# Kernel optimization log

Hardware: AMD Instinct MI355X
Metric: run time of the kernel (lower is better)

## Reference

```python
import jax, jax.numpy as jnp
import numpy as np

L, B, D, H, M, F = 384, 16, 1024, 16, 64, 4096
HD = D // H
LEFT, RIGHT = 64, 64
STD_SCALE = 0.5
LN_EPS = 1e-5


def layer_norm(x, w, b):
    mu = jnp.mean(x, axis=-1, keepdims=True)
    var = jnp.mean((x - mu) ** 2, axis=-1, keepdims=True)
    return (x - mu) / jnp.sqrt(var + LN_EPS) * w + b


def linear(x, w, b):  # torch nn.Linear: y = x @ W^T + b, w is [out, in]
    return x @ w.T + b


def attention_suppression(aw, scale):
    # aw: [N, Tq, Tk] raw logits (may contain -inf)
    p = jax.nn.softmax(aw, axis=-1)
    nz = p > 0.0  # entries with -inf logits are exactly 0 after softmax
    nzs = jnp.sum(nz.astype(aw.dtype), axis=-1, keepdims=True)
    mean = jnp.sum(p, axis=-1, keepdims=True) / nzs
    dis = jnp.where(nz, (p - mean) ** 2, jnp.zeros_like(p))
    var = jnp.sum(dis, axis=-1, keepdims=True) / (nzs - 1.0)
    thr = mean - scale * jnp.sqrt(var)
    return jnp.where(p < thr, -jnp.inf, aw)


def setup_inputs() -> dict:
    key = jax.random.key(0)
    ks = jax.random.split(key, 24)
    s = 0.02

    def w(k, shape):
        return jax.random.normal(k, shape, dtype=jnp.float32) * s

    return {
        "x": jax.random.normal(ks[0], (L, B, D), dtype=jnp.float32),
        "memory": jax.random.normal(ks[1], (M, B, D), dtype=jnp.float32),
        "q_w": w(ks[2], (D, D)), "q_b": jnp.zeros((D,), jnp.float32),
        "k_w": w(ks[3], (D, D)), "k_b": jnp.zeros((D,), jnp.float32),
        "v_w": w(ks[4], (D, D)), "v_b": jnp.zeros((D,), jnp.float32),
        "out_w": w(ks[5], (D, D)), "out_b": jnp.zeros((D,), jnp.float32),
        "ln1_w": jnp.ones((D,), jnp.float32), "ln1_b": jnp.zeros((D,), jnp.float32),
        "fc1_w": w(ks[6], (F, D)), "fc1_b": jnp.zeros((F,), jnp.float32),
        "fc2_w": w(ks[7], (D, F)), "fc2_b": jnp.zeros((D,), jnp.float32),
        "ln2_w": jnp.ones((D,), jnp.float32), "ln2_b": jnp.zeros((D,), jnp.float32),
    }


def reference(x, memory, q_w, q_b, k_w, k_b, v_w, v_b, out_w, out_b,
              ln1_w, ln1_b, fc1_w, fc1_b, fc2_w, fc2_b, ln2_w, ln2_b):
    residual = x
    xn = layer_norm(x, ln1_w, ln1_b)  # normalize_before
    # summarization query = mean over segment (excluding left/right context)
    summary = jnp.mean(xn[LEFT:L - RIGHT], axis=0, keepdims=True)  # [1,B,D]
    inp = jnp.concatenate([xn, summary], axis=0)  # [L+1, B, D]
    mem_and_inp = jnp.concatenate([memory, inp[:-1]], axis=0)  # [M+L, B, D]

    scaling = HD ** -0.5
    q = linear(inp, q_w, q_b) * scaling
    k = linear(mem_and_inp, k_w, k_b)
    v = linear(mem_and_inp, v_w, v_b)

    def split_heads(t):  # [T,B,D] -> [B*H, T, HD]
        return t.reshape(t.shape[0], B * H, HD).transpose(1, 0, 2)

    q, k, v = split_heads(q), split_heads(k), split_heads(v)
    aw = jnp.einsum('nqd,nkd->nqk', q, k)  # [B*H, L+1, M+L]
    # disable mem-on-mem: summary (last) query must not attend to memory keys
    aw = aw.at[:, -1, :M].set(-jnp.inf)
    aw = attention_suppression(aw, STD_SCALE)
    p = jax.nn.softmax(aw, axis=-1)
    attn = jnp.einsum('nqk,nkd->nqd', p, v)  # [B*H, L+1, HD]
    attn = attn.transpose(1, 0, 2).reshape(L + 1, B, D)
    out_and_mem = linear(attn, out_w, out_b)
    # next_m = out_and_mem[-1:] appended to state (identity squash); output drops it
    out = out_and_mem[:-1]

    x = residual + out
    residual = x
    xn = layer_norm(x, ln2_w, ln2_b)
    h = jax.nn.relu(linear(xn, fc1_w, fc1_b))
    h = linear(h, fc2_w, fc2_b)
    return residual + h
```

## Files before the change

### kernel.cpp

```cpp
#include <hip/hip_runtime.h>

typedef __bf16 bf16x8 __attribute__((ext_vector_type(8)));
typedef float f32x4 __attribute__((ext_vector_type(4)));
typedef unsigned short u16x8 __attribute__((ext_vector_type(8)));

__device__ __forceinline__ unsigned short f2bf(float f) {
  union { float f; unsigned int u; } v; v.f = f;
  unsigned int r = v.u + 0x7fffu + ((v.u >> 16) & 1u);
  return (unsigned short)(r >> 16);
}

__device__ __forceinline__ void async16(const unsigned short* g, unsigned short* l) {
  __builtin_amdgcn_global_load_lds(
      (const __attribute__((address_space(1))) unsigned int*)g,
      (__attribute__((address_space(3))) unsigned int*)l, 16, 0, 0);
}

__global__ void cvt_all(const float* __restrict__ q_w, const float* __restrict__ k_w,
                        const float* __restrict__ v_w, const float* __restrict__ o_w,
                        const float* __restrict__ f1w, const float* __restrict__ f2w,
                        const float* __restrict__ mem,
                        const float* __restrict__ q_b, const float* __restrict__ k_b,
                        const float* __restrict__ v_b,
                        unsigned short* __restrict__ WQ, unsigned short* __restrict__ WK,
                        unsigned short* __restrict__ WV, unsigned short* __restrict__ WO,
                        unsigned short* __restrict__ WF1, unsigned short* __restrict__ WF2,
                        unsigned short* __restrict__ MEMB, float* __restrict__ QKVB) {
  const int bid = blockIdx.x;
  const float* src; unsigned short* dst; float scale = 1.f; int base;
  if (bid < 1024)       { src = q_w; dst = WQ;  scale = 0.125f; base = 0; }
  else if (bid < 2048)  { src = k_w; dst = WK;  base = 1024; }
  else if (bid < 3072)  { src = v_w; dst = WV;  base = 2048; }
  else if (bid < 4096)  { src = o_w; dst = WO;  base = 3072; }
  else if (bid < 8192)  { src = f1w; dst = WF1; base = 4096; }
  else if (bid < 12288) { src = f2w; dst = WF2; base = 8192; }
  else if (bid < 13312) { src = mem; dst = MEMB; base = 12288; }
  else {
    const int i = (bid - 13312) * 256 + threadIdx.x;
    QKVB[i] = (i < 1024) ? q_b[i] * 0.125f : (i < 2048 ? k_b[i - 1024] : v_b[i - 2048]);
    return;
  }
  const int i = (bid - base) * 256 + threadIdx.x;
  float4 v = ((const float4*)src)[i];
  ushort4 o;
  o.x = f2bf(v.x * scale); o.y = f2bf(v.y * scale);
  o.z = f2bf(v.z * scale); o.w = f2bf(v.w * scale);
  ((ushort4*)dst)[i] = o;
}

template <int PREFILL>
__global__ __launch_bounds__(256) void ln_bf16(
    const float* __restrict__ src, unsigned short* __restrict__ dst,
    const float* __restrict__ g, const float* __restrict__ be,
    const float* __restrict__ fbias, float* __restrict__ dout) {
  const int row = blockIdx.x, tid = threadIdx.x;
  const float4 v = ((const float4*)(src + (size_t)row * 1024))[tid];
  if (PREFILL) {
    const float4 fb = ((const float4*)fbias)[tid];
    float4 r;
    r.x = v.x + fb.x; r.y = v.y + fb.y; r.z = v.z + fb.z; r.w = v.w + fb.w;
    ((float4*)(dout + (size_t)row * 1024))[tid] = r;
  }
  float s = v.x + v.y + v.z + v.w;
  float qq = v.x * v.x + v.y * v.y + v.z * v.z + v.w * v.w;
#pragma unroll
  for (int off = 32; off; off >>= 1) { s += __shfl_xor(s, off); qq += __shfl_xor(qq, off); }
  __shared__ float ps[4], pq[4];
  const int w = tid >> 6, lane = tid & 63;
  if (lane == 0) { ps[w] = s; pq[w] = qq; }
  __syncthreads();
  if (tid == 0) { ps[0] = ps[0] + ps[1] + ps[2] + ps[3]; pq[0] = pq[0] + pq[1] + pq[2] + pq[3]; }
  __syncthreads();
  const float mu = ps[0] * (1.f / 1024.f);
  const float var = pq[0] * (1.f / 1024.f) - mu * mu;
  const float rs = rsqrtf(var + 1e-5f);
  const float4 gv = ((const float4*)g)[tid];
  const float4 bv = ((const float4*)be)[tid];
  ushort4 o;
  o.x = f2bf((v.x - mu) * rs * gv.x + bv.x);
  o.y = f2bf((v.y - mu) * rs * gv.y + bv.y);
  o.z = f2bf((v.z - mu) * rs * gv.z + bv.z);
  o.w = f2bf((v.w - mu) * rs * gv.w + bv.w);
  ((ushort4*)(dst + (size_t)row * 1024))[tid] = o;
}

#define KOFF 6291456ull
#define VOFF 13631488ull
template <int EPI>
__global__ __launch_bounds__(256) void gemm_bt(
    const unsigned short* __restrict__ A, const unsigned short* __restrict__ Bw,
    const float* __restrict__ bias, const float* __restrict__ resid,
    void* __restrict__ Cout, int M, int N, int K, int lda, int ldb, int NBN, int WM) {
  __shared__ __align__(16) unsigned short lA[128 * 32];
  __shared__ __align__(16) unsigned short lB[128 * 32];
  const int tid = threadIdx.x;
  const int w = tid >> 6, lane = tid & 63;
  const int lr = lane & 15, lq = lane >> 4;
  const int l = blockIdx.x;
  const int xcd = l & 7, r = l >> 3;
  const int bm = xcd * WM + (r % WM);
  const int rest = r / WM;
  const int bn = rest % NBN;
  const size_t koff = (size_t)(rest / NBN) * K;
  const unsigned short* Ab = A + (size_t)bm * 128 * lda + koff;
  const unsigned short* Bb = Bw + (size_t)bn * 128 * ldb + koff;
  const int wm = (w & 1) << 6, wn = (w >> 1) << 6;
  f32x4 acc[4][4] = {};
  const int kiters = K >> 5;
  const int c0 = tid, c1 = 256 + tid;
  const int r0 = c0 >> 2, o0 = (c0 & 3) << 3;
  const int r1 = c1 >> 2, o1 = (c1 & 3) << 3;
  for (int kt = 0; kt < kiters; ++kt) {
    const int kb = kt << 5;
    __syncthreads();
    async16(Ab + (size_t)r0 * lda + kb + o0, lA + c0 * 8);
    async16(Bb + (size_t)r0 * ldb + kb + o0, lB + c0 * 8);
    async16(Ab + (size_t)r1 * lda + kb + o1, lA + c1 * 8);
    async16(Bb + (size_t)r1 * ldb + kb + o1, lB + c1 * 8);
    __syncthreads();
    bf16x8 af[4], bfr[4];
#pragma unroll
    for (int i = 0; i < 4; ++i) af[i] = *(const bf16x8*)(lA + (wm + i * 16 + lr) * 32 + lq * 8);
#pragma unroll
    for (int i = 0; i < 4; ++i) bfr[i] = *(const bf16x8*)(lB + (wn + i * 16 + lr) * 32 + lq * 8);
#pragma unroll
    for (int i = 0; i < 4; ++i)
#pragma unroll
      for (int j = 0; j < 4; ++j)
        acc[i][j] = __builtin_amdgcn_mfma_f32_16x16x32_bf16(af[i], bfr[j], acc[i][j], 0, 0, 0);
  }
  const int which = (bn * 128) >> 10;
#pragma unroll
  for (int i = 0; i < 4; ++i) {
#pragma unroll
    for (int j = 0; j < 4; ++j) {
      const int colg = bn * 128 + wn + j * 16 + lr;
      const float bi = (EPI == 6) ? 0.f : bias[colg];
      const int rowg0 = bm * 128 + wm + i * 16 + lq * 4;
#pragma unroll
      for (int r2 = 0; r2 < 4; ++r2) {
        const int rowg = rowg0 + r2;
        const float val = acc[i][j][r2] + bi;
        if (EPI == 5) {
          const int t = rowg >> 4, bb = rowg & 15;
          const int hh = (colg >> 6) & 15, dd = colg & 63;
          const size_t nn = (size_t)(bb * 16 + hh);
          unsigned short* q16 = (unsigned short*)Cout;
          if (which == 0) {
            if (rowg >= 1024) q16[(nn * 384 + (t - 64)) * 64 + dd] = f2bf(val);
          } else if (which == 1) {
            q16[KOFF + (nn * 448 + t) * 64 + dd] = f2bf(val);
          } else {
            q16[VOFF + (nn * 448 + t) * 64 + dd] = f2bf(val);
          }
        } else {
          const size_t idx = (size_t)rowg * N + colg;
          if (EPI == 2) ((float*)Cout)[idx] = val + resid[idx];
          else if (EPI == 3) ((unsigned short*)Cout)[idx] = f2bf(fmaxf(val, 0.f));
          else if (EPI == 6) atomicAdd(&((float*)Cout)[idx], acc[i][j][r2]);
        }
      }
    }
  }
}

__global__ __launch_bounds__(256) void vtrans(const unsigned short* __restrict__ vb,
                                              unsigned short* __restrict__ vt) {
  __shared__ __align__(16) unsigned short ls[64][80];
  const int kc = blockIdx.x, n = blockIdx.y;
  const int tid = threadIdx.x;
#pragma unroll
  for (int i = 0; i < 2; ++i) {
    const int c = i * 256 + tid;
    const int kk = c >> 3, dc = (c & 7) << 3;
    u16x8 val = *(const u16x8*)(vb + ((size_t)n * 448 + kc * 64 + kk) * 64 + dc);
    *(u16x8*)&ls[kk][dc] = val;
  }
  __syncthreads();
#pragma unroll
  for (int i = 0; i < 2; ++i) {
    const int c = i * 256 + tid;
    const int d = c >> 3, kx = (c & 7) << 3;
    u16x8 o;
#pragma unroll
    for (int j = 0; j < 8; ++j) o[j] = ls[kx + j][d];
    *(u16x8*)(vt + ((size_t)n * 64 + d) * 448 + kc * 64 + kx) = o;
  }
}

#define PST 468
__global__ __launch_bounds__(256) void attn_kernel(
    const unsigned short* __restrict__ qt_, const unsigned short* __restrict__ kt_,
    const unsigned short* __restrict__ vt_, unsigned short* __restrict__ attn) {
  __shared__ __align__(16) unsigned short P[16 * PST];
  __shared__ float Rm[4][16], Rs[4][16], Rc[4][16], Rv[4][16], R2[4][16];
  __shared__ __align__(16) float OT[4][16][17];
  const int id = blockIdx.x;
  const int xcd = id & 7, j0 = id >> 3;
  const int n = xcd * 32 + (j0 & 31), qt = j0 >> 5;
  const int b = n >> 4, h = n & 15;
  const int tid = threadIdx.x, w = tid >> 6, lane = tid & 63;
  const int lr = lane & 15, lq = lane >> 4;

  const unsigned short* qp = qt_ + ((size_t)n * 384 + qt * 16 + lr) * 64 + lq * 8;
  const bf16x8 q0 = *(const bf16x8*)qp;
  const bf16x8 q1 = *(const bf16x8*)(qp + 32);

  f32x4 acc[7];
#pragma unroll
  for (int t = 0; t < 7; ++t) {
    const unsigned short* kp = kt_ + ((size_t)n * 448 + (w * 7 + t) * 16 + lr) * 64 + lq * 8;
    const bf16x8 k0 = *(const bf16x8*)kp;
    const bf16x8 k1 = *(const bf16x8*)(kp + 32);
    f32x4 a = {0.f, 0.f, 0.f, 0.f};
    a = __builtin_amdgcn_mfma_f32_16x16x32_bf16(k0, q0, a, 0, 0, 0);
    a = __builtin_amdgcn_mfma_f32_16x16x32_bf16(k1, q1, a, 0, 0, 0);
    acc[t] = a;
  }

  f32x4 m4 = acc[0];
#pragma unroll
  for (int t = 1; t < 7; ++t) {
    m4[0] = fmaxf(m4[0], acc[t][0]); m4[1] = fmaxf(m4[1], acc[t][1]);
    m4[2] = fmaxf(m4[2], acc[t][2]); m4[3] = fmaxf(m4[3], acc[t][3]);
  }
  float m = fmaxf(fmaxf(m4[0], m4[1]), fmaxf(m4[2], m4[3]));
  m = fmaxf(m, __shfl_xor(m, 16));
  m = fmaxf(m, __shfl_xor(m, 32));
  if (lq == 0) Rm[w][lr] = m;
  __syncthreads();
  m = fmaxf(fmaxf(Rm[0][lr], Rm[1][lr]), fmaxf(Rm[2][lr], Rm[3][lr]));

  f32x4 s4 = {0.f, 0.f, 0.f, 0.f}, c4 = {0.f, 0.f, 0.f, 0.f};
#pragma unroll
  for (int t = 0; t < 7; ++t) {
#pragma unroll
    for (int r = 0; r < 4; ++r) {
      const float e = __expf(acc[t][r] - m);
      acc[t][r] = e;
      s4[r] += e;
      if (e > 0.f) c4[r] += 1.f;
    }
  }
  float s = (s4[0] + s4[1]) + (s4[2] + s4[3]);
  float cnt = (c4[0] + c4[1]) + (c4[2] + c4[3]);
  s += __shfl_xor(s, 16); s += __shfl_xor(s, 32);
  cnt += __shfl_xor(cnt, 16); cnt += __shfl_xor(cnt, 32);
  if (lq == 0) { Rs[w][lr] = s; Rc[w][lr] = cnt; }
  __syncthreads();
  s = (Rs[0][lr] + Rs[1][lr]) + (Rs[2][lr] + Rs[3][lr]);
  cnt = (Rc[0][lr] + Rc[1][lr]) + (Rc[2][lr] + Rc[3][lr]);
  const float inv = 1.f / s;
  const float mean = 1.f / cnt;

  f32x4 d4 = {0.f, 0.f, 0.f, 0.f};
#pragma unroll
  for (int t = 0; t < 7; ++t) {
#pragma unroll
    for (int r = 0; r < 4; ++r) {
      const float p = acc[t][r] * inv;
      const float dd = p - mean;
      if (acc[t][r] > 0.f) d4[r] += dd * dd;
    }
  }
  float dv = (d4[0] + d4[1]) + (d4[2] + d4[3]);
  dv += __shfl_xor(dv, 16); dv += __shfl_xor(dv, 32);
  if (lq == 0) Rv[w][lr] = dv;
  __syncthreads();
  dv = (Rv[0][lr] + Rv[1][lr]) + (Rv[2][lr] + Rv[3][lr]);
  const float thr = mean - 0.5f * sqrtf(dv / (cnt - 1.f));

  f32x4 t4 = {0.f, 0.f, 0.f, 0.f};
#pragma unroll
  for (int t = 0; t < 7; ++t) {
#pragma unroll
    for (int r = 0; r < 4; ++r) {
      if (!(acc[t][r] * inv < thr)) t4[r] += acc[t][r];
    }
  }
  float s2 = (t4[0] + t4[1]) + (t4[2] + t4[3]);
  s2 += __shfl_xor(s2, 16); s2 += __shfl_xor(s2, 32);
  if (lq == 0) R2[w][lr] = s2;
  __syncthreads();
  s2 = (R2[0][lr] + R2[1][lr]) + (R2[2][lr] + R2[3][lr]);
  const float inv2 = 1.f / s2;

#pragma unroll
  for (int t = 0; t < 7; ++t) {
#pragma unroll
    for (int rp = 0; rp < 4; rp += 2) {
      const float v0 = (acc[t][rp] * inv < thr) ? 0.f : acc[t][rp] * inv2;
      const float v1 = (acc[t][rp + 1] * inv < thr) ? 0.f : acc[t][rp + 1] * inv2;
      const unsigned int u = (unsigned int)f2bf(v0) | ((unsigned int)f2bf(v1) << 16);
      *(unsigned int*)&P[lr * PST + (w * 7 + t) * 16 + lq * 4 + rp] = u;
    }
  }
  __syncthreads();

  f32x4 o = {0.f, 0.f, 0.f, 0.f};
#pragma unroll
  for (int c = 0; c < 14; ++c) {
    union { ushort4 hh[2]; bf16x8 v; } bf;
    bf.hh[0] = *(const ushort4*)&P[lr * PST + c * 32 + lq * 8];
    bf.hh[1] = *(const ushort4*)&P[lr * PST + c * 32 + lq * 8 + 4];
    const bf16x8 a = *(const bf16x8*)(vt_ + ((size_t)n * 64 + w * 16 + lr) * 448 + c * 32 + lq * 8);
    o = __builtin_amdgcn_mfma_f32_16x16x32_bf16(a, bf.v, o, 0, 0, 0);
  }

#pragma unroll
  for (int r = 0; r < 4; ++r) OT[w][lq * 4 + r][lr] = o[r];
  const int qrow = lane >> 2, dg = lane & 3;
  ushort4 ov;
  ov.x = f2bf(OT[w][dg * 4 + 0][qrow]);
  ov.y = f2bf(OT[w][dg * 4 + 1][qrow]);
  ov.z = f2bf(OT[w][dg * 4 + 2][qrow]);
  ov.w = f2bf(OT[w][dg * 4 + 3][qrow]);
  *(ushort4*)(attn + ((size_t)(qt * 16 + qrow) * 16 + b) * 1024 + h * 64 + w * 16 + dg * 4) = ov;
}

extern "C" void kernel_launch(void* const* d_in, const int* in_sizes, int n_in,
                              void* d_out, int out_size, void* d_ws, size_t ws_size,
                              hipStream_t stream) {
  (void)in_sizes; (void)n_in; (void)out_size; (void)ws_size;
  const float* x    = (const float*)d_in[0];
  const float* mem  = (const float*)d_in[1];
  const float* q_w  = (const float*)d_in[2];
  const float* q_b  = (const float*)d_in[3];
  const float* k_w  = (const float*)d_in[4];
  const float* k_b  = (const float*)d_in[5];
  const float* v_w  = (const float*)d_in[6];
  const float* v_b  = (const float*)d_in[7];
  const float* o_w  = (const float*)d_in[8];
  const float* o_b  = (const float*)d_in[9];
  const float* ln1w = (const float*)d_in[10];
  const float* ln1b = (const float*)d_in[11];
  const float* f1w  = (const float*)d_in[12];
  const float* f1b  = (const float*)d_in[13];
  const float* f2w  = (const float*)d_in[14];
  const float* f2b  = (const float*)d_in[15];
  const float* ln2w = (const float*)d_in[16];
  const float* ln2b = (const float*)d_in[17];

  unsigned short* WQ   = (unsigned short*)d_ws;
  unsigned short* WK   = WQ + 1048576;
  unsigned short* WV   = WK + 1048576;
  unsigned short* WO   = WV + 1048576;
  unsigned short* WF1  = WO + 1048576;
  unsigned short* WF2  = WF1 + 4194304;
  unsigned short* ABUF = WF2 + 4194304;
  unsigned short* QB   = ABUF + 7340032;
  unsigned short* KB   = QB + 6291456;
  unsigned short* VB   = KB + 7340032;
  unsigned short* VT   = VB + 7340032;
  unsigned short* ATTN = VT + 7340032;
  float*          X2   = (float*)(ATTN + 6291456);
  float*          QKVB = (float*)ATTN;
  unsigned short* XN2  = ATTN;
  unsigned short* HB   = ABUF;

  cvt_all<<<13324, 256, 0, stream>>>(q_w, k_w, v_w, o_w, f1w, f2w, mem, q_b, k_b, v_b,
                                     WQ, WK, WV, WO, WF1, WF2, ABUF, QKVB);

  ln_bf16<0><<<6144, 256, 0, stream>>>(x, ABUF + 1048576, ln1w, ln1b, nullptr, nullptr);

  gemm_bt<5><<<1344, 256, 0, stream>>>(ABUF, WQ, QKVB, nullptr, QB, 7168, 3072, 1024, 1024, 1024, 24, 7);

  vtrans<<<dim3(7, 256), 256, 0, stream>>>(VB, VT);
  attn_kernel<<<6144, 256, 0, stream>>>(QB, KB, VT, ATTN);

  gemm_bt<2><<<384, 256, 0, stream>>>(ATTN, WO, o_b, x, X2, 6144, 1024, 1024, 1024, 1024, 8, 6);

  ln_bf16<1><<<6144, 256, 0, stream>>>(X2, XN2, ln2w, ln2b, f2b, (float*)d_out);

  gemm_bt<3><<<1536, 256, 0, stream>>>(XN2, WF1, f1b, nullptr, HB, 6144, 4096, 1024, 1024, 1024, 32, 6);
  gemm_bt<6><<<768, 256, 0, stream>>>(HB, WF2, nullptr, nullptr, d_out, 6144, 1024, 2048, 4096, 4096, 8, 6);
}
```

Baseline: 521.6 us.

## Replace FC1 GEMM with 256x256-tile 8-wave pipelined MFMA kernel

Adds a dedicated FC1+ReLU GEMM kernel using 512 threads, 256x256 output tiles, double-buffered async global-to-LDS loads, and an explicitly interleaved schedule of LDS reads, staging and MFMA with priority hints and manual waitcnts. It also maps tiles to XCDs so each XCD works on contiguous row blocks. The goal is higher MFMA utilisation and better operand reuse on the largest GEMM than the generic gemm_bt path gives. In exchange it uses more LDS and registers per block (launch bounds cap it at 2 blocks per CU), and the hand-tuned wait counts are fragile.

```diff
diff --git a/kernel.cpp b/kernel.cpp
--- a/kernel.cpp
+++ b/kernel.cpp
@@ -164,6 +164,121 @@
   }
 }
 
+#define WAITV10() asm volatile("s_waitcnt vmcnt(10)" ::: "memory")
+#define WAITV8()  asm volatile("s_waitcnt vmcnt(8)" ::: "memory")
+#define WAITV0()  asm volatile("s_waitcnt vmcnt(0)" ::: "memory")
+#define WAITL0()  asm volatile("s_waitcnt lgkmcnt(0)" ::: "memory")
+#define BAR()     do { __builtin_amdgcn_s_barrier(); __builtin_amdgcn_sched_barrier(0); } while (0)
+#define SCHED()   __builtin_amdgcn_sched_barrier(0)
+
+#define STG_A(bufv, ksv, ktv) do { \
+    unsigned short* d_ = (unsigned short*)lA8 + (bufv) * 16384 + (ksv) * 8192; \
+    const unsigned short* s_ = Ab + (((ktv) << 6) + ((ksv) << 5)); \
+    async16(s_ + (size_t)sr0 * lda + sc0, d_ + ci0 * 8); \
+    async16(s_ + (size_t)sr1 * lda + sc1, d_ + ci1 * 8); } while (0)
+#define STG_B(bufv, ksv, ktv) do { \
+    unsigned short* d_ = (unsigned short*)lB8 + (bufv) * 16384 + (ksv) * 8192; \
+    const unsigned short* s_ = Bb + (((ktv) << 6) + ((ksv) << 5)); \
+    async16(s_ + (size_t)sr0 * ldb + sc0, d_ + ci0 * 8); \
+    async16(s_ + (size_t)sr1 * ldb + sc1, d_ + ci1 * 8); } while (0)
+#define RD_A4(dst, bufv, ksv, mh) \
+  _Pragma("unroll") \
+  for (int i = 0; i < 4; ++i) \
+    dst[i] = *(const bf16x8*)((unsigned short*)lA8 + (bufv) * 16384 + (ksv) * 8192 + \
+                              (wm * 128 + (mh) * 64 + i * 16 + lr) * 32 + lq * 8)
+#define RD_B4(dst, bufv, ksv) \
+  _Pragma("unroll") \
+  for (int j = 0; j < 4; ++j) \
+    dst[j] = *(const bf16x8*)((unsigned short*)lB8 + (bufv) * 16384 + (ksv) * 8192 + \
+                              (wn * 64 + j * 16 + lr) * 32 + lq * 8)
+#define MFMA16(accbase, av, bv) \
+  _Pragma("unroll") \
+  for (int i = 0; i < 4; ++i) \
+  _Pragma("unroll") \
+  for (int j = 0; j < 4; ++j) \
+    acc[(accbase) + i][j] = \
+        __builtin_amdgcn_mfma_f32_16x16x32_bf16(av[i], bv[j], acc[(accbase) + i][j], 0, 0, 0)
+
+__global__ __launch_bounds__(512, 2) void gemm8_relu(
+    const unsigned short* __restrict__ A, const unsigned short* __restrict__ Bw,
+    const float* __restrict__ bias, unsigned short* __restrict__ Cout,
+    int N, int lda, int ldb, int MT) {
+  __shared__ __align__(16) unsigned short lA8[32768];
+  __shared__ __align__(16) unsigned short lB8[32768];
+  const int tid = threadIdx.x;
+  const int w = tid >> 6, lane = tid & 63;
+  const int wm = w >> 2, wn = w & 3;
+  const int lr = lane & 15, lq = lane >> 4;
+  const int bid = blockIdx.x;
+  const int xcd = bid & 7, r = bid >> 3;
+  const int bm = xcd * MT + (r % MT);
+  const int bn = r / MT;
+  const unsigned short* Ab = A + (size_t)bm * 256 * lda;
+  const unsigned short* Bb = Bw + (size_t)bn * 256 * ldb;
+  const int ci0 = tid, ci1 = tid + 512;
+  const int sr0 = ci0 >> 2, sc0 = (ci0 & 3) << 3;
+  const int sr1 = ci1 >> 2, sc1 = (ci1 & 3) << 3;
+
+  f32x4 acc[8][4] = {};
+  bf16x8 aP[4], aN[4], b0[4], b1[4];
+
+  STG_B(0, 0, 0); STG_A(0, 0, 0); STG_B(0, 1, 0); STG_A(0, 1, 0);
+  STG_B(1, 0, 1); STG_A(1, 0, 1); STG_B(1, 1, 1); STG_A(1, 1, 1);
+  WAITV8();
+  BAR();
+  RD_A4(aP, 0, 0, 0);
+  RD_B4(b0, 0, 0);
+
+  for (int kt = 0; kt < 16; ++kt) {
+    const int buf = kt & 1, nbuf = buf ^ 1, kt2 = kt + 2;
+    const bool st = kt2 < 16, tail = kt >= 14;
+    WAITL0(); if (tail) { WAITV0(); } else { WAITV10(); } BAR();
+    if (st) STG_B(buf, 0, kt2);
+    RD_A4(aN, buf, 0, 1);
+    SCHED();
+    __builtin_amdgcn_s_setprio(1);
+    MFMA16(0, aP, b0);
+    __builtin_amdgcn_s_setprio(0);
+    WAITL0(); if (tail) { WAITV0(); } else { WAITV10(); } BAR();
+    if (st) STG_A(buf, 0, kt2);
+    RD_A4(aP, buf, 1, 0);
+    RD_B4(b1, buf, 1);
+    SCHED();
+    __builtin_amdgcn_s_setprio(1);
+    MFMA16(4, aN, b0);
+    __builtin_amdgcn_s_setprio(0);
+    WAITL0(); if (tail) { WAITV0(); } else { WAITV10(); } BAR();
+    if (st) STG_B(buf, 1, kt2);
+    RD_A4(aN, buf, 1, 1);
+    SCHED();
+    __builtin_amdgcn_s_setprio(1);
+    MFMA16(0, aP, b1);
+    __builtin_amdgcn_s_setprio(0);
+    WAITL0(); if (tail) { WAITV0(); } else { WAITV10(); } BAR();
+    if (st) STG_A(buf, 1, kt2);
+    if (kt < 15) { RD_A4(aP, nbuf, 0, 0); RD_B4(b0, nbuf, 0); }
+    SCHED();
+    __builtin_amdgcn_s_setprio(1);
+    MFMA16(4, aN, b1);
+    __builtin_amdgcn_s_setprio(0);
+  }
+
+#pragma unroll
+  for (int j = 0; j < 4; ++j) {
+    const int colg = bn * 256 + wn * 64 + j * 16 + lr;
+    const float bi = bias[colg];
+#pragma unroll
+    for (int i = 0; i < 8; ++i) {
+      const int rowg0 = bm * 256 + wm * 128 + i * 16 + lq * 4;
+#pragma unroll
+      for (int r2 = 0; r2 < 4; ++r2) {
+        const float v = acc[i][j][r2] + bi;
+        Cout[(size_t)(rowg0 + r2) * N + colg] = f2bf(fmaxf(v, 0.f));
+      }
+    }
+  }
+}
+
 __global__ __launch_bounds__(256) void vtrans(const unsigned short* __restrict__ vb,
                                               unsigned short* __restrict__ vt) {
   __shared__ __align__(16) unsigned short ls[64][80];
@@ -372,6 +487,6 @@
 
   ln_bf16<1><<<6144, 256, 0, stream>>>(X2, XN2, ln2w, ln2b, f2b, (float*)d_out);
 
-  gemm_bt<3><<<1536, 256, 0, stream>>>(XN2, WF1, f1b, nullptr, HB, 6144, 4096, 1024, 1024, 1024, 32, 6);
+  gemm8_relu<<<384, 512, 0, stream>>>(XN2, WF1, f1b, HB, 4096, 1024, 1024, 3);
   gemm_bt<6><<<768, 256, 0, stream>>>(HB, WF2, nullptr, nullptr, d_out, 6144, 1024, 2048, 4096, 4096, 8, 6);
 }
```

Measured after the change: 548.2 us. +5.1%, slower.
